# Kernel tuning notes

Hardware: AMD Instinct MI355X
Metric: run time of the kernel (lower is better)

The kernel has to match this reference:

```python
import jax, jax.numpy as jnp
import numpy as np

N_NODES = 50000
N_EDGES = 1600000
D_IN = 1028
D_OUT = 256
NEG_SLOPE = 0.2


def setup_inputs() -> dict:
    key = jax.random.key(0)
    ks = jax.random.split(key, 6)
    x = jax.random.normal(ks[0], (N_NODES, D_IN), dtype=jnp.float32)
    edge_index = jax.random.randint(ks[1], (2, N_EDGES), 0, N_NODES, dtype=jnp.int64)
    # GATv2Conv params (heads=1): separate source/target linear maps, attention vector, bias
    W_l = jax.random.normal(ks[2], (D_IN, D_OUT), dtype=jnp.float32) / np.sqrt(D_IN)
    W_r = jax.random.normal(ks[3], (D_IN, D_OUT), dtype=jnp.float32) / np.sqrt(D_IN)
    att = jax.random.normal(ks[4], (D_OUT,), dtype=jnp.float32) / np.sqrt(D_OUT)
    bias = jax.random.normal(ks[5], (D_OUT,), dtype=jnp.float32) * 0.01
    return {"x": x, "edge_index": edge_index, "W_l": W_l, "W_r": W_r, "att": att, "bias": bias}


def reference(x, edge_index, W_l, W_r, att, bias):
    # Single-layer GATv2Conv(1028 -> 256, heads=1, add_self_loops=True)
    n = x.shape[0]
    xl = x @ W_l  # source-side features [N, D_OUT]
    xr = x @ W_r  # target-side features [N, D_OUT]
    loops = jnp.arange(n, dtype=edge_index.dtype)
    src = jnp.concatenate([edge_index[0], loops])  # [E + N]
    dst = jnp.concatenate([edge_index[1], loops])
    # e_ij = a . LeakyReLU(xl[j] + xr[i])
    e = jax.nn.leaky_relu(xl[src] + xr[dst], NEG_SLOPE) @ att  # [E + N]
    # softmax over incoming edges per destination node (self-loops guarantee nonempty segments)
    emax = jax.ops.segment_max(e, dst, num_segments=n)
    p = jnp.exp(e - emax[dst])
    denom = jax.ops.segment_sum(p, dst, num_segments=n)
    alpha = p / denom[dst]  # [E + N]
    out = jax.ops.segment_sum(alpha[:, None] * xl[src], dst, num_segments=n)
    return out + bias
```

## Files before the change

kernel.cpp:

```cpp
#include <hip/hip_runtime.h>
#include <hip/hip_bf16.h>
#include <stdint.h>


#define N_NODES 50000
#define N_EDGES 1600000
#define D_IN    1028
#define KPAD    1056
#define D_OUT   256
#define NB      512

typedef __bf16 bf16x8 __attribute__((ext_vector_type(8)));
typedef float  f32x4  __attribute__((ext_vector_type(4)));

static __device__ __forceinline__ void gl_lds16(const void* g, void* l) {
  __builtin_amdgcn_global_load_lds(
      (const __attribute__((address_space(1))) unsigned int*)g,
      (__attribute__((address_space(3))) unsigned int*)l, 16, 0, 0);
}
static __device__ __forceinline__ float bf2f(unsigned short u) {
  union { unsigned int i; float f; } c; c.i = ((unsigned int)u) << 16; return c.f;
}
static __device__ __forceinline__ unsigned short f2bf(float f) {
  union { float f; unsigned int i; } c; c.f = f;
  unsigned int r = 0x7fffu + ((c.i >> 16) & 1u);
  return (unsigned short)((c.i + r) >> 16);
}

__global__ void k_mode(const unsigned int* __restrict__ ei32, int* __restrict__ mode) {
  int t = blockIdx.x * 256 + threadIdx.x;
  if (t < 2048 && ei32[2 * t + 1] != 0u) atomicOr(mode, 1);
}

__global__ void k_x2b(const float* __restrict__ x, unsigned short* __restrict__ xb) {
  long long idx = (long long)blockIdx.x * 256 + threadIdx.x;
  if (idx >= (long long)N_NODES * KPAD) return;
  int n = (int)(idx / KPAD);
  int k = (int)(idx - (long long)n * KPAD);
  xb[idx] = (k < D_IN) ? f2bf(x[(size_t)n * D_IN + k]) : (unsigned short)0;
}

__global__ void k_wt(const float* __restrict__ Wl, const float* __restrict__ Wr,
                     unsigned short* __restrict__ Wt) {
  int idx = blockIdx.x * 256 + threadIdx.x;
  if (idx >= NB * KPAD) return;
  int k = idx / NB;
  int n = idx - k * NB;
  unsigned short v = 0;
  if (k < D_IN) v = f2bf((n < D_OUT) ? Wl[k * D_OUT + n] : Wr[k * D_OUT + (n - D_OUT)]);
  Wt[(size_t)n * KPAD + k] = v;
}

__global__ __launch_bounds__(256) void k_gemm(const unsigned short* __restrict__ xb,
                                              const unsigned short* __restrict__ Wt,
                                              unsigned short* __restrict__ xf, int M) {
  __shared__ unsigned short As[128 * 32];
  __shared__ unsigned short Bs[128 * 32];
  const int tid = threadIdx.x;
  const int w = tid >> 6, lane = tid & 63;
  const int m0 = blockIdx.x * 128, n0 = blockIdx.y * 128;
  const int wm = (w >> 1) * 64, wn = (w & 1) * 64;

  f32x4 zero = {0.f, 0.f, 0.f, 0.f};
  f32x4 acc[4][4];
#pragma unroll
  for (int i = 0; i < 4; ++i)
#pragma unroll
    for (int j = 0; j < 4; ++j) acc[i][j] = zero;

  const int lrow = lane >> 2, lch = lane & 3;

  for (int k0 = 0; k0 < KPAD; k0 += 32) {
    __syncthreads();
#pragma unroll
    for (int j = 0; j < 2; ++j) {
      int gm = m0 + w * 32 + j * 16 + lrow;
      if (gm >= M) gm = M - 1;
      const char* g = (const char*)xb + ((size_t)gm * KPAD + k0) * 2 + lch * 16;
      gl_lds16(g, &As[(w * 32 + j * 16) * 32]);
    }
#pragma unroll
    for (int j = 0; j < 2; ++j) {
      int gn = n0 + w * 32 + j * 16 + lrow;
      const char* g = (const char*)Wt + ((size_t)gn * KPAD + k0) * 2 + lch * 16;
      gl_lds16(g, &Bs[(w * 32 + j * 16) * 32]);
    }
    __syncthreads();

    bf16x8 af[4], bfr[4];
#pragma unroll
    for (int t = 0; t < 4; ++t)
      af[t] = *(const bf16x8*)&As[(wm + t * 16 + (lane & 15)) * 32 + (lane >> 4) * 8];
#pragma unroll
    for (int t = 0; t < 4; ++t)
      bfr[t] = *(const bf16x8*)&Bs[(wn + t * 16 + (lane & 15)) * 32 + (lane >> 4) * 8];
#pragma unroll
    for (int mt = 0; mt < 4; ++mt)
#pragma unroll
      for (int nt = 0; nt < 4; ++nt)
        acc[mt][nt] = __builtin_amdgcn_mfma_f32_16x16x32_bf16(af[mt], bfr[nt], acc[mt][nt], 0, 0, 0);
  }

  const int col = lane & 15, rq = (lane >> 4) * 4;
#pragma unroll
  for (int mt = 0; mt < 4; ++mt)
#pragma unroll
    for (int nt = 0; nt < 4; ++nt)
#pragma unroll
      for (int r = 0; r < 4; ++r) {
        int m = m0 + wm + mt * 16 + rq + r;
        if (m < M) xf[(size_t)m * NB + (n0 + wn + nt * 16 + col)] = f2bf(acc[mt][nt][r]);
      }
}

static __device__ __forceinline__ int load_idx(const int* ei, const long long* ei64,
                                               int md, int pos, int n) {
  int v = md ? ei[pos] : (int)ei64[pos];
  v = v < 0 ? 0 : (v >= n ? n - 1 : v);
  return v;
}

__global__ void k_hist(const int* __restrict__ ei, const int* __restrict__ mode,
                       int E, int* __restrict__ deg, int n) {
  int e = blockIdx.x * blockDim.x + threadIdx.x;
  if (e < E) {
    int d = load_idx(ei, (const long long*)ei, *mode, E + e, n);
    atomicAdd(&deg[d], 1);
  }
}

__global__ void k_scan(const int* __restrict__ deg, int* __restrict__ rowstart,
                       int* __restrict__ cursor, int n) {
  __shared__ int wsum[16];
  __shared__ int woff[16];
  __shared__ int running_sh;
  if (threadIdx.x == 0) running_sh = 0;
  __syncthreads();
  for (int start = 0; start < n; start += 1024) {
    int i = start + (int)threadIdx.x;
    int v = (i < n) ? deg[i] : 0;
    int x = v;
#pragma unroll
    for (int off = 1; off < 64; off <<= 1) {
      int y = __shfl_up(x, off, 64);
      if ((int)(threadIdx.x & 63) >= off) x += y;
    }
    if ((threadIdx.x & 63) == 63) wsum[threadIdx.x >> 6] = x;
    __syncthreads();
    if (threadIdx.x == 0) {
      int a = running_sh;
      for (int wv = 0; wv < 16; ++wv) { woff[wv] = a; a += wsum[wv]; }
      running_sh = a;
    }
    __syncthreads();
    int excl = woff[threadIdx.x >> 6] + (x - v);
    if (i < n) { rowstart[i] = excl; cursor[i] = excl; }
    __syncthreads();
  }
  if (threadIdx.x == 0) rowstart[n] = running_sh;
}

__global__ void k_scatter(const int* __restrict__ ei, const int* __restrict__ mode,
                          int E, int* __restrict__ cursor, int* __restrict__ ssrc, int n) {
  int e = blockIdx.x * blockDim.x + threadIdx.x;
  if (e < E) {
    int md = *mode;
    int s = load_idx(ei, (const long long*)ei, md, e, n);
    int d = load_idx(ei, (const long long*)ei, md, E + e, n);
    int pos = atomicAdd(&cursor[d], 1);
    if (pos >= 0 && pos < E) ssrc[pos] = s;
  }
}

static __device__ __forceinline__ float4 load_bf4(const unsigned short* p) {
  ushort4 u = *(const ushort4*)p;
  float4 f; f.x = bf2f(u.x); f.y = bf2f(u.y); f.z = bf2f(u.z); f.w = bf2f(u.w);
  return f;
}
static __device__ __forceinline__ float edge_e(float4 v, float4 xr, float4 a) {
  float t0 = v.x + xr.x; t0 = t0 > 0.f ? t0 : 0.2f * t0;
  float t1 = v.y + xr.y; t1 = t1 > 0.f ? t1 : 0.2f * t1;
  float t2 = v.z + xr.z; t2 = t2 > 0.f ? t2 : 0.2f * t2;
  float t3 = v.w + xr.w; t3 = t3 > 0.f ? t3 : 0.2f * t3;
  float p = fmaf(a.x, t0, fmaf(a.y, t1, fmaf(a.z, t2, a.w * t3)));
#pragma unroll
  for (int off = 32; off > 0; off >>= 1) p += __shfl_xor(p, off, 64);
  return p;
}

__global__ __launch_bounds__(256) void k_gat(const unsigned short* __restrict__ xf,
    const int* __restrict__ rowstart, const int* __restrict__ ssrc,
    const float* __restrict__ att, const float* __restrict__ bias,
    float* __restrict__ out, int n) {
  const int gw = (int)((blockIdx.x * blockDim.x + threadIdx.x) >> 6);
  const int lane = (int)(threadIdx.x & 63);
  if (gw >= n) return;

  const float4 a = ((const float4*)att)[lane];
  float4 xr = load_bf4(xf + (size_t)gw * NB + D_OUT + 4 * lane);

  float4 xl = load_bf4(xf + (size_t)gw * NB + 4 * lane);
  float m = edge_e(xl, xr, a);
  float l = 1.f;
  float4 acc = xl;

  const int beg = rowstart[gw], end = rowstart[gw + 1];
  for (int i = beg; i < end; ++i) {
    int s = ssrc[i];
    s = s < 0 ? 0 : (s >= n ? n - 1 : s);
    float4 v = load_bf4(xf + (size_t)s * NB + 4 * lane);
    float e = edge_e(v, xr, a);
    float mn = fmaxf(m, e);
    float sc = __expf(m - mn);
    float p  = __expf(e - mn);
    acc.x = acc.x * sc + p * v.x;
    acc.y = acc.y * sc + p * v.y;
    acc.z = acc.z * sc + p * v.z;
    acc.w = acc.w * sc + p * v.w;
    l = l * sc + p;
    m = mn;
  }

  float inv = 1.f / l;
  const float4 b = ((const float4*)bias)[lane];
  float4 o;
  o.x = fmaf(acc.x, inv, b.x);
  o.y = fmaf(acc.y, inv, b.y);
  o.z = fmaf(acc.z, inv, b.z);
  o.w = fmaf(acc.w, inv, b.w);
  ((float4*)out)[(size_t)gw * 64 + lane] = o;
}

extern "C" void kernel_launch(void* const* d_in, const int* in_sizes, int n_in,
                              void* d_out, int out_size, void* d_ws, size_t ws_size,
                              hipStream_t stream) {
  (void)in_sizes; (void)n_in; (void)out_size; (void)ws_size;
  const float* x   = (const float*)d_in[0];
  const int*   ei  = (const int*)d_in[1];
  const float* Wl  = (const float*)d_in[2];
  const float* Wr  = (const float*)d_in[3];
  const float* att = (const float*)d_in[4];
  const float* bia = (const float*)d_in[5];
  float* out = (float*)d_out;

  const int N = N_NODES;
  const int E = N_EDGES;

  char* ws = (char*)d_ws;
  size_t off = 0;
  unsigned short* xb = (unsigned short*)(ws + off); off += (size_t)N * KPAD * 2;
  unsigned short* xf = (unsigned short*)(ws + off); off += (size_t)N * NB * 2;
  unsigned short* Wt = (unsigned short*)(ws + off); off += (size_t)NB * KPAD * 2;
  off = (off + 255) & ~(size_t)255;
  int* deg      = (int*)(ws + off); off += (size_t)N * 4;
  int* rowstart = (int*)(ws + off); off += (size_t)(N + 1) * 4;
  off = (off + 255) & ~(size_t)255;
  int* cursor   = (int*)(ws + off); off += (size_t)N * 4;
  int* ssrc     = (int*)(ws + off); off += (size_t)E * 4;
  off = (off + 255) & ~(size_t)255;
  int* mode     = (int*)(ws + off); off += 256;

  hipMemsetAsync(deg, 0, (size_t)N * 4, stream);
  hipMemsetAsync(mode, 0, 4, stream);
  k_mode<<<8, 256, 0, stream>>>((const unsigned int*)ei, mode);
  {
    long long tot = (long long)N * KPAD;
    k_x2b<<<(unsigned)((tot + 255) / 256), 256, 0, stream>>>(x, xb);
  }
  k_wt<<<(NB * KPAD + 255) / 256, 256, 0, stream>>>(Wl, Wr, Wt);
  k_gemm<<<dim3((N + 127) / 128, NB / 128), 256, 0, stream>>>(xb, Wt, xf, N);
  k_hist<<<(E + 255) / 256, 256, 0, stream>>>(ei, mode, E, deg, N);
  k_scan<<<1, 1024, 0, stream>>>(deg, rowstart, cursor, N);
  k_scatter<<<(E + 255) / 256, 256, 0, stream>>>(ei, mode, E, cursor, ssrc, N);
  k_gat<<<(N + 3) / 4, 256, 0, stream>>>(xf, rowstart, ssrc, att, bia, out, N);
}
```

Before: 889.2 us.

## Batch GAT edge gathers by eight, fuse prep kernels, and rewrite scan

Unrolls the per-destination aggregation to load eight neighbor rows at once and applies the online softmax per batch, so more gather loads are in flight. It also fuses the x-to-bf16 conversion (now vectorized, one block per row), the weight transpose and the degree histogram into one launch. The block-serial scan is replaced with a per-thread segmented scan, and the two memsets are merged. Padding edges add some wasted work for low-degree nodes and increase register pressure.

```diff
diff --git a/kernel.cpp b/kernel.cpp
--- a/kernel.cpp
+++ b/kernel.cpp
@@ -10,6 +10,11 @@
 #define D_OUT   256
 #define NB      512
 
+#define X2B_BLOCKS  N_NODES
+#define WT_BLOCKS   ((NB * KPAD + 255) / 256)
+#define HIST_BLOCKS ((N_EDGES + 255) / 256)
+#define PREP_BLOCKS (X2B_BLOCKS + WT_BLOCKS + HIST_BLOCKS)
+
 typedef __bf16 bf16x8 __attribute__((ext_vector_type(8)));
 typedef float  f32x4  __attribute__((ext_vector_type(4)));
 
@@ -32,23 +37,47 @@
   if (t < 2048 && ei32[2 * t + 1] != 0u) atomicOr(mode, 1);
 }
 
-__global__ void k_x2b(const float* __restrict__ x, unsigned short* __restrict__ xb) {
-  long long idx = (long long)blockIdx.x * 256 + threadIdx.x;
-  if (idx >= (long long)N_NODES * KPAD) return;
-  int n = (int)(idx / KPAD);
-  int k = (int)(idx - (long long)n * KPAD);
-  xb[idx] = (k < D_IN) ? f2bf(x[(size_t)n * D_IN + k]) : (unsigned short)0;
-}
-
-__global__ void k_wt(const float* __restrict__ Wl, const float* __restrict__ Wr,
-                     unsigned short* __restrict__ Wt) {
-  int idx = blockIdx.x * 256 + threadIdx.x;
-  if (idx >= NB * KPAD) return;
-  int k = idx / NB;
-  int n = idx - k * NB;
-  unsigned short v = 0;
-  if (k < D_IN) v = f2bf((n < D_OUT) ? Wl[k * D_OUT + n] : Wr[k * D_OUT + (n - D_OUT)]);
-  Wt[(size_t)n * KPAD + k] = v;
+static __device__ __forceinline__ int load_idx(const int* ei, int md, int pos, int n) {
+  int v = md ? ei[pos] : (int)((const long long*)ei)[pos];
+  return v < 0 ? 0 : (v >= n ? n - 1 : v);
+}
+
+__global__ __launch_bounds__(256) void k_prep(const float* __restrict__ x,
+    const float* __restrict__ Wl, const float* __restrict__ Wr,
+    const int* __restrict__ ei, const int* __restrict__ mode,
+    unsigned short* __restrict__ xb, unsigned short* __restrict__ Wt,
+    int* __restrict__ deg) {
+  const int b = blockIdx.x, t = threadIdx.x;
+  if (b < X2B_BLOCKS) {
+    const float* xr = x + (size_t)b * D_IN;
+    unsigned short* xo = xb + (size_t)b * KPAD;
+    float4 v = *(const float4*)(xr + 4 * t);
+    ushort4 o; o.x = f2bf(v.x); o.y = f2bf(v.y); o.z = f2bf(v.z); o.w = f2bf(v.w);
+    *(ushort4*)(xo + 4 * t) = o;
+    if (t == 0) {
+      float4 v2 = *(const float4*)(xr + 1024);
+      ushort4 o2; o2.x = f2bf(v2.x); o2.y = f2bf(v2.y); o2.z = f2bf(v2.z); o2.w = f2bf(v2.w);
+      *(ushort4*)(xo + 1024) = o2;
+    } else if (t < 8) {
+      ushort4 z = {0, 0, 0, 0};
+      *(ushort4*)(xo + 1024 + 4 * t) = z;
+    }
+  } else if (b < X2B_BLOCKS + WT_BLOCKS) {
+    int idx = (b - X2B_BLOCKS) * 256 + t;
+    if (idx < NB * KPAD) {
+      int k = idx / NB;
+      int n = idx - k * NB;
+      unsigned short v = 0;
+      if (k < D_IN) v = f2bf((n < D_OUT) ? Wl[k * D_OUT + n] : Wr[k * D_OUT + (n - D_OUT)]);
+      Wt[(size_t)n * KPAD + k] = v;
+    }
+  } else {
+    int e = (b - X2B_BLOCKS - WT_BLOCKS) * 256 + t;
+    if (e < N_EDGES) {
+      int d = load_idx(ei, *mode, N_EDGES + e, N_NODES);
+      atomicAdd(&deg[d], 1);
+    }
+  }
 }
 
 __global__ __launch_bounds__(256) void k_gemm(const unsigned short* __restrict__ xb,
@@ -113,62 +142,52 @@
       }
 }
 
-static __device__ __forceinline__ int load_idx(const int* ei, const long long* ei64,
-                                               int md, int pos, int n) {
-  int v = md ? ei[pos] : (int)ei64[pos];
-  v = v < 0 ? 0 : (v >= n ? n - 1 : v);
-  return v;
-}
-
-__global__ void k_hist(const int* __restrict__ ei, const int* __restrict__ mode,
-                       int E, int* __restrict__ deg, int n) {
+__global__ __launch_bounds__(1024) void k_scan(const int* __restrict__ deg,
+    int* __restrict__ rowstart, int* __restrict__ cursor, int n) {
+  const int t = (int)threadIdx.x;
+  const int lane = t & 63, wid = t >> 6;
+  const int seg = (n + 1023) / 1024;
+  const int base = t * seg;
+  __shared__ int wsum[16];
+
+  int sum = 0;
+  for (int j = 0; j < seg; ++j) { int i = base + j; if (i < n) sum += deg[i]; }
+
+  int x = sum;
+#pragma unroll
+  for (int off = 1; off < 64; off <<= 1) {
+    int y = __shfl_up(x, off, 64);
+    if (lane >= off) x += y;
+  }
+  if (lane == 63) wsum[wid] = x;
+  __syncthreads();
+  if (t < 16) {
+    int v = wsum[t], s = v;
+#pragma unroll
+    for (int off = 1; off < 16; off <<= 1) {
+      int y = __shfl_up(s, off, 16);
+      if (t >= off) s += y;
+    }
+    wsum[t] = s - v;
+  }
+  __syncthreads();
+  int run = wsum[wid] + (x - sum);
+  for (int j = 0; j < seg; ++j) {
+    int i = base + j;
+    if (i < n) { rowstart[i] = run; cursor[i] = run; run += deg[i]; }
+  }
+  if (t == 1023) rowstart[n] = run;
+}
+
+__global__ void k_scatter(const int* __restrict__ ei, const int* __restrict__ mode,
+                          int* __restrict__ cursor, int* __restrict__ ssrc) {
   int e = blockIdx.x * blockDim.x + threadIdx.x;
-  if (e < E) {
-    int d = load_idx(ei, (const long long*)ei, *mode, E + e, n);
-    atomicAdd(&deg[d], 1);
-  }
-}
-
-__global__ void k_scan(const int* __restrict__ deg, int* __restrict__ rowstart,
-                       int* __restrict__ cursor, int n) {
-  __shared__ int wsum[16];
-  __shared__ int woff[16];
-  __shared__ int running_sh;
-  if (threadIdx.x == 0) running_sh = 0;
-  __syncthreads();
-  for (int start = 0; start < n; start += 1024) {
-    int i = start + (int)threadIdx.x;
-    int v = (i < n) ? deg[i] : 0;
-    int x = v;
-#pragma unroll
-    for (int off = 1; off < 64; off <<= 1) {
-      int y = __shfl_up(x, off, 64);
-      if ((int)(threadIdx.x & 63) >= off) x += y;
-    }
-    if ((threadIdx.x & 63) == 63) wsum[threadIdx.x >> 6] = x;
-    __syncthreads();
-    if (threadIdx.x == 0) {
-      int a = running_sh;
-      for (int wv = 0; wv < 16; ++wv) { woff[wv] = a; a += wsum[wv]; }
-      running_sh = a;
-    }
-    __syncthreads();
-    int excl = woff[threadIdx.x >> 6] + (x - v);
-    if (i < n) { rowstart[i] = excl; cursor[i] = excl; }
-    __syncthreads();
-  }
-  if (threadIdx.x == 0) rowstart[n] = running_sh;
-}
-
-__global__ void k_scatter(const int* __restrict__ ei, const int* __restrict__ mode,
-                          int E, int* __restrict__ cursor, int* __restrict__ ssrc, int n) {
-  int e = blockIdx.x * blockDim.x + threadIdx.x;
-  if (e < E) {
+  if (e < N_EDGES) {
     int md = *mode;
-    int s = load_idx(ei, (const long long*)ei, md, e, n);
-    int d = load_idx(ei, (const long long*)ei, md, E + e, n);
+    int s = load_idx(ei, md, e, N_NODES);
+    int d = load_idx(ei, md, N_EDGES + e, N_NODES);
     int pos = atomicAdd(&cursor[d], 1);
-    if (pos >= 0 && pos < E) ssrc[pos] = s;
+    if (pos >= 0 && pos < N_EDGES) ssrc[pos] = s;
   }
 }
 
@@ -177,22 +196,19 @@
   float4 f; f.x = bf2f(u.x); f.y = bf2f(u.y); f.z = bf2f(u.z); f.w = bf2f(u.w);
   return f;
 }
-static __device__ __forceinline__ float edge_e(float4 v, float4 xr, float4 a) {
+static __device__ __forceinline__ float part4(float4 v, float4 xr, float4 a) {
   float t0 = v.x + xr.x; t0 = t0 > 0.f ? t0 : 0.2f * t0;
   float t1 = v.y + xr.y; t1 = t1 > 0.f ? t1 : 0.2f * t1;
   float t2 = v.z + xr.z; t2 = t2 > 0.f ? t2 : 0.2f * t2;
   float t3 = v.w + xr.w; t3 = t3 > 0.f ? t3 : 0.2f * t3;
-  float p = fmaf(a.x, t0, fmaf(a.y, t1, fmaf(a.z, t2, a.w * t3)));
-#pragma unroll
-  for (int off = 32; off > 0; off >>= 1) p += __shfl_xor(p, off, 64);
-  return p;
+  return fmaf(a.x, t0, fmaf(a.y, t1, fmaf(a.z, t2, a.w * t3)));
 }
 
 __global__ __launch_bounds__(256) void k_gat(const unsigned short* __restrict__ xf,
     const int* __restrict__ rowstart, const int* __restrict__ ssrc,
     const float* __restrict__ att, const float* __restrict__ bias,
     float* __restrict__ out, int n) {
-  const int gw = (int)((blockIdx.x * blockDim.x + threadIdx.x) >> 6);
+  const int gw = (int)blockIdx.x * 4 + (int)(threadIdx.x >> 6);
   const int lane = (int)(threadIdx.x & 63);
   if (gw >= n) return;
 
@@ -200,24 +216,57 @@
   float4 xr = load_bf4(xf + (size_t)gw * NB + D_OUT + 4 * lane);
 
   float4 xl = load_bf4(xf + (size_t)gw * NB + 4 * lane);
-  float m = edge_e(xl, xr, a);
+  float m;
+  {
+    float p = part4(xl, xr, a);
+#pragma unroll
+    for (int off = 32; off > 0; off >>= 1) p += __shfl_xor(p, off, 64);
+    m = p;
+  }
   float l = 1.f;
   float4 acc = xl;
 
-  const int beg = rowstart[gw], end = rowstart[gw + 1];
-  for (int i = beg; i < end; ++i) {
-    int s = ssrc[i];
-    s = s < 0 ? 0 : (s >= n ? n - 1 : s);
-    float4 v = load_bf4(xf + (size_t)s * NB + 4 * lane);
-    float e = edge_e(v, xr, a);
-    float mn = fmaxf(m, e);
+  const int end = rowstart[gw + 1];
+  for (int i = rowstart[gw]; i < end; i += 8) {
+    float4 v[8];
+    float pe[8];
+#pragma unroll
+    for (int j = 0; j < 8; ++j) {
+      int idx = i + j;
+      int sj = (idx < end) ? ssrc[idx] : gw;
+      sj = sj < 0 ? 0 : (sj >= n ? n - 1 : sj);
+      v[j] = load_bf4(xf + (size_t)sj * NB + 4 * lane);
+    }
+#pragma unroll
+    for (int j = 0; j < 8; ++j) pe[j] = part4(v[j], xr, a);
+#pragma unroll
+    for (int off = 32; off > 0; off >>= 1)
+#pragma unroll
+      for (int j = 0; j < 8; ++j) pe[j] += __shfl_xor(pe[j], off, 64);
+#pragma unroll
+    for (int j = 0; j < 8; ++j) if (i + j >= end) pe[j] = -1e30f;
+
+    float mb = pe[0];
+#pragma unroll
+    for (int j = 1; j < 8; ++j) mb = fmaxf(mb, pe[j]);
+    float mn = fmaxf(m, mb);
     float sc = __expf(m - mn);
-    float p  = __expf(e - mn);
-    acc.x = acc.x * sc + p * v.x;
-    acc.y = acc.y * sc + p * v.y;
-    acc.z = acc.z * sc + p * v.z;
-    acc.w = acc.w * sc + p * v.w;
-    l = l * sc + p;
+    float psum = 0.f;
+    float4 va = {0.f, 0.f, 0.f, 0.f};
+#pragma unroll
+    for (int j = 0; j < 8; ++j) {
+      float p = __expf(pe[j] - mn);
+      psum += p;
+      va.x = fmaf(p, v[j].x, va.x);
+      va.y = fmaf(p, v[j].y, va.y);
+      va.z = fmaf(p, v[j].z, va.z);
+      va.w = fmaf(p, v[j].w, va.w);
+    }
+    acc.x = fmaf(acc.x, sc, va.x);
+    acc.y = fmaf(acc.y, sc, va.y);
+    acc.z = fmaf(acc.z, sc, va.z);
+    acc.w = fmaf(acc.w, sc, va.w);
+    l = fmaf(l, sc, psum);
     m = mn;
   }
 
@@ -253,24 +302,17 @@
   unsigned short* Wt = (unsigned short*)(ws + off); off += (size_t)NB * KPAD * 2;
   off = (off + 255) & ~(size_t)255;
   int* deg      = (int*)(ws + off); off += (size_t)N * 4;
+  int* mode     = (int*)(ws + off); off += 256;
   int* rowstart = (int*)(ws + off); off += (size_t)(N + 1) * 4;
   off = (off + 255) & ~(size_t)255;
   int* cursor   = (int*)(ws + off); off += (size_t)N * 4;
   int* ssrc     = (int*)(ws + off); off += (size_t)E * 4;
-  off = (off + 255) & ~(size_t)255;
-  int* mode     = (int*)(ws + off); off += 256;
-
-  hipMemsetAsync(deg, 0, (size_t)N * 4, stream);
-  hipMemsetAsync(mode, 0, 4, stream);
+
+  hipMemsetAsync(deg, 0, (size_t)N * 4 + 256, stream);
   k_mode<<<8, 256, 0, stream>>>((const unsigned int*)ei, mode);
-  {
-    long long tot = (long long)N * KPAD;
-    k_x2b<<<(unsigned)((tot + 255) / 256), 256, 0, stream>>>(x, xb);
-  }
-  k_wt<<<(NB * KPAD + 255) / 256, 256, 0, stream>>>(Wl, Wr, Wt);
+  k_prep<<<PREP_BLOCKS, 256, 0, stream>>>(x, Wl, Wr, ei, mode, xb, Wt, deg);
   k_gemm<<<dim3((N + 127) / 128, NB / 128), 256, 0, stream>>>(xb, Wt, xf, N);
-  k_hist<<<(E + 255) / 256, 256, 0, stream>>>(ei, mode, E, deg, N);
   k_scan<<<1, 1024, 0, stream>>>(deg, rowstart, cursor, N);
-  k_scatter<<<(E + 255) / 256, 256, 0, stream>>>(ei, mode, E, cursor, ssrc, N);
+  k_scatter<<<(E + 255) / 256, 256, 0, stream>>>(ei, mode, cursor, ssrc);
   k_gat<<<(N + 3) / 4, 256, 0, stream>>>(xf, rowstart, ssrc, att, bia, out, N);
 }
```

New measurement: 960.7 us. 1.08x slower.
